# Performance work log

Hardware: AMD Instinct MI355X
Metric: run time of the kernel (lower is better)

Reference implementation:

```python
import jax, jax.numpy as jnp
import numpy as np

EMBED = 256
HEADS = 8
LEVELS = 4
POINTS = 4
HEAD_DIM = EMBED // HEADS
SHAPES = [(100, 100), (50, 50), (25, 25), (13, 13)]  # (H, W) per level
NUM_KEYS = sum(h * w for h, w in SHAPES)  # 13294
LEVEL_STARTS = np.cumsum([0] + [h * w for h, w in SHAPES])[:-1]
B, Q = 8, 900


def _offset_bias():
    # Faithful reproduction of the torch _reset_parameters sampling_offsets bias.
    th = np.arange(HEADS, dtype=np.float32) * (2.0 * np.pi / HEADS)
    g = np.stack([np.cos(th), np.sin(th)], -1)
    g = g / np.abs(g).max(-1, keepdims=True)
    g = np.tile(g[:, None, None, :], (1, LEVELS, POINTS, 1))
    g = g * np.arange(1, POINTS + 1, dtype=np.float32)[None, None, :, None]
    return jnp.asarray(g.reshape(-1), dtype=jnp.float32)


def setup_inputs() -> dict:
    key = jax.random.key(0)
    ks = jax.random.split(key, 12)
    s = 1.0 / np.sqrt(EMBED)
    return {
        "query": jax.random.normal(ks[0], (B, Q, EMBED), jnp.float32),
        "reference_points": jax.random.uniform(ks[1], (B, Q, LEVELS, 2), jnp.float32),
        "value": jax.random.normal(ks[2], (B, NUM_KEYS, EMBED), jnp.float32),
        "spatial_shapes": jnp.asarray(np.array(SHAPES, dtype=np.int32)),
        "level_start_index": jnp.asarray(LEVEL_STARTS.astype(np.int32)),
        "W_off": jax.random.normal(ks[3], (EMBED, HEADS * LEVELS * POINTS * 2), jnp.float32) * 0.01,
        "b_off": _offset_bias(),
        "W_attn": jax.random.normal(ks[4], (EMBED, HEADS * LEVELS * POINTS), jnp.float32) * 0.01,
        "b_attn": jnp.zeros((HEADS * LEVELS * POINTS,), jnp.float32),
        "W_val": jax.random.normal(ks[5], (EMBED, EMBED), jnp.float32) * s,
        "b_val": jnp.zeros((EMBED,), jnp.float32),
        "W_out": jax.random.normal(ks[6], (EMBED, EMBED), jnp.float32) * s,
        "b_out": jnp.zeros((EMBED,), jnp.float32),
    }


def _bilinear(vflat, x, y, H, W):
    # vflat: [BH, H*W, D]; x, y: [BH, Q, P] in unnormalized pixel coords.
    # grid_sample(mode='bilinear', padding_mode='zeros', align_corners=False)
    BH, Qn, Pn = x.shape
    D = vflat.shape[-1]
    x0f = jnp.floor(x); y0f = jnp.floor(y)
    wx = x - x0f; wy = y - y0f
    x0 = x0f.astype(jnp.int32); y0 = y0f.astype(jnp.int32)

    def gather(xi, yi):
        inb = (xi >= 0) & (xi < W) & (yi >= 0) & (yi < H)
        idx = jnp.clip(yi, 0, H - 1) * W + jnp.clip(xi, 0, W - 1)
        g = jnp.take_along_axis(vflat, idx.reshape(BH, Qn * Pn, 1), axis=1)
        return g.reshape(BH, Qn, Pn, D) * inb[..., None].astype(vflat.dtype)

    v00 = gather(x0, y0)
    v01 = gather(x0 + 1, y0)
    v10 = gather(x0, y0 + 1)
    v11 = gather(x0 + 1, y0 + 1)
    return (v00 * ((1 - wx) * (1 - wy))[..., None]
            + v01 * (wx * (1 - wy))[..., None]
            + v10 * ((1 - wx) * wy)[..., None]
            + v11 * (wx * wy)[..., None])


def _msda(value_hd, shapes_np, starts_np, loc, attw):
    # value_hd: [B, K, H, D]; loc: [B, Q, H, L, P, 2]; attw: [B, Q, H, L, P]
    Bn, K, Hn, D = value_hd.shape
    Qn, Pn = loc.shape[1], loc.shape[4]
    out = jnp.zeros((Bn * Hn, Qn, D), value_hd.dtype)
    for l, (Hl, Wl) in enumerate(shapes_np):
        s = int(starts_np[l])
        v = value_hd[:, s:s + Hl * Wl]                      # [B, Hl*Wl, H, D]
        v = v.reshape(Bn, Hl * Wl, Hn, D).transpose(0, 2, 1, 3)
        vflat = v.reshape(Bn * Hn, Hl * Wl, D)
        # sampling_grid = 2*loc - 1; grid_sample align_corners=False -> x = loc*W - 0.5
        lx = loc[:, :, :, l, :, 0].transpose(0, 2, 1, 3).reshape(Bn * Hn, Qn, Pn)
        ly = loc[:, :, :, l, :, 1].transpose(0, 2, 1, 3).reshape(Bn * Hn, Qn, Pn)
        samp = _bilinear(vflat, lx * Wl - 0.5, ly * Hl - 0.5, Hl, Wl)  # [BH,Q,P,D]
        w = attw[:, :, :, l, :].transpose(0, 2, 1, 3).reshape(Bn * Hn, Qn, Pn)
        out = out + jnp.einsum('bqpd,bqp->bqd', samp, w)
    return out.reshape(Bn, Hn, Qn, D).transpose(0, 2, 1, 3).reshape(Bn, Qn, Hn * D)


def reference(query, reference_points, value, spatial_shapes, level_start_index,
              W_off, b_off, W_attn, b_attn, W_val, b_val, W_out, b_out):
    shapes_np = np.asarray(spatial_shapes)
    starts_np = np.asarray(level_start_index)
    Bn, Qn, _ = query.shape
    K = value.shape[1]

    v = value @ W_val + b_val                              # [B, K, E]
    v = v.reshape(Bn, K, HEADS, HEAD_DIM)

    off = (query @ W_off + b_off).reshape(Bn, Qn, HEADS, LEVELS, POINTS, 2)
    aw = (query @ W_attn + b_attn).reshape(Bn, Qn, HEADS, LEVELS * POINTS)
    aw = jax.nn.softmax(aw, axis=-1).reshape(Bn, Qn, HEADS, LEVELS, POINTS)

    # offset_normalizer = (W, H) per level
    norm = jnp.asarray(shapes_np[:, ::-1].astype(np.float32)).reshape(1, 1, 1, LEVELS, 1, 2)
    loc = reference_points[:, :, None, :, None, :] + off / norm  # [B,Q,H,L,P,2]

    out = _msda(v, shapes_np, starts_np, loc, aw)          # [B, Q, E]
    return out @ W_out + b_out
```

## Files before the change

kernel.cpp:

```cpp
#include <hip/hip_runtime.h>
#include <hip/hip_bf16.h>
#include <math.h>
#include <type_traits>

#define BATCH 8
#define QLEN 900
#define HEADS 8
#define LEVELS 4
#define POINTS 4
#define NUM_KEYS 13294
#define BQ (BATCH * QLEN)
#define MROWS_V (BATCH * NUM_KEYS)
#define VTILES (MROWS_V / 16)
#define VBLOCKS 512
#define TPB 13

__constant__ const int c_LH[4] = {100, 50, 25, 13};
__constant__ const int c_LW[4] = {100, 50, 25, 13};
__constant__ const int c_LS[4] = {0, 10000, 12500, 13125};

typedef __attribute__((ext_vector_type(8))) short bfrag;
typedef __attribute__((ext_vector_type(4))) float ffrag;

static __device__ __forceinline__ unsigned short f2bf(float f) {
    __hip_bfloat16 h = __float2bfloat16(f);
    return *(unsigned short*)&h;
}
static __device__ __forceinline__ float bf2f(unsigned int u16) {
    unsigned int v = u16 << 16;
    float f;
    __builtin_memcpy(&f, &v, 4);
    return f;
}
static __device__ __forceinline__ unsigned long long pack4bf(float4 v) {
    return (unsigned long long)f2bf(v.x)
         | ((unsigned long long)f2bf(v.y) << 16)
         | ((unsigned long long)f2bf(v.z) << 32)
         | ((unsigned long long)f2bf(v.w) << 48);
}

__global__ __launch_bounds__(256)
void prep_kernel(const float* __restrict__ W_val, const float* __restrict__ W_off,
                 const float* __restrict__ W_attn, const float* __restrict__ W_out,
                 const float* __restrict__ b_off, const float* __restrict__ b_attn,
                 unsigned short* __restrict__ Wv, unsigned short* __restrict__ Woa,
                 unsigned short* __restrict__ Wo, float* __restrict__ boa) {
    const int id = blockIdx.x * 256 + threadIdx.x;
    if (id < 65536) {
        const int n = id >> 8, k = id & 255;
        Wv[id] = f2bf(W_val[k * 256 + n]);
    } else if (id < 131072) {
        const int t = id - 65536;
        const int n = t >> 8, k = t & 255;
        Woa[t] = f2bf(W_off[k * 256 + n]);
    } else if (id < 163840) {
        const int t = id - 131072;
        const int n = t >> 8, k = t & 255;
        Woa[65536 + t] = f2bf(W_attn[k * 128 + n]);
    } else if (id < 229376) {
        const int t = id - 163840;
        const int n = t >> 8, k = t & 255;
        Wo[t] = f2bf(W_out[k * 256 + n]);
    } else if (id < 229760) {
        const int t = id - 229376;
        boa[t] = (t < 256) ? b_off[t] : b_attn[t - 256];
    }
}

#define VSTEP(T, LREG)                                                        \
  do {                                                                        \
    const char* abuf = (const char*)&Abuf[0][0] + rb * 8192;                  \
    ffrag acc[2];                                                             \
    _Pragma("unroll")                                                         \
    for (int j_ = 0; j_ < 2; ++j_) acc[j_] = (ffrag){0.f, 0.f, 0.f, 0.f};     \
    _Pragma("unroll")                                                         \
    for (int ks_ = 0; ks_ < 8; ++ks_) {                                       \
      const int ub_ = (ks_ * 64 + quad * 16) ^ ((ln & 7) << 4);               \
      const bfrag af_ = *(const bfrag*)(abuf + ln * 512 + ub_);               \
      _Pragma("unroll")                                                       \
      for (int j_ = 0; j_ < 2; ++j_)                                          \
        acc[j_] = __builtin_amdgcn_mfma_f32_16x16x32_bf16(af_, b[j_][ks_],    \
                                                          acc[j_], 0, 0, 0); \
    }                                                                         \
    if ((T) + 1 < t1) {                                                       \
      const int wb_ = (rb + 1 == 3) ? 0 : rb + 1;                             \
      char* dbuf_ = (char*)&Abuf[0][0] + wb_ * 8192;                          \
      _Pragma("unroll")                                                       \
      for (int i_ = 0; i_ < 2; ++i_)                                          \
        *(unsigned long long*)(dbuf_ + dsoff[i_]) = pack4bf(LREG[i_]);        \
      if ((T) + 3 < t1) {                                                     \
        const float4* ap_ = Af4 + (size_t)((T) + 3) * 1024 + tid;             \
        _Pragma("unroll")                                                     \
        for (int i_ = 0; i_ < 2; ++i_) LREG[i_] = ap_[i_ * 512];              \
      }                                                                       \
    }                                                                         \
    const int rowb_ = (T) * 16 + quad * 4;                                    \
    _Pragma("unroll")                                                         \
    for (int r_ = 0; r_ < 4; ++r_) {                                          \
      const unsigned row_ = rowb_ + r_;                                       \
      const unsigned bb_ = row_ / NUM_KEYS;                                   \
      const unsigned key_ = row_ - bb_ * NUM_KEYS;                            \
      _Pragma("unroll")                                                       \
      for (int j_ = 0; j_ < 2; ++j_) {                                        \
        const int col_ = n0 + j_ * 16 + ln;                                   \
        const int h_ = col_ >> 5, d_ = col_ & 31;                             \
        C[((size_t)(bb_ * 8 + h_) * NUM_KEYS + key_) * 32 + d_] =             \
            f2bf(acc[j_][r_] + bj[j_]);                                       \
      }                                                                       \
    }                                                                         \
    asm volatile("s_waitcnt lgkmcnt(0)" ::: "memory");                        \
    __builtin_amdgcn_s_barrier();                                             \
    rb = (rb + 1 == 3) ? 0 : rb + 1;                                          \
  } while (0)

__global__ __launch_bounds__(512, 4)
void gemm_val_stream(const float* __restrict__ A, const unsigned short* __restrict__ WT,
                     const float* __restrict__ bias, unsigned short* __restrict__ C) {
    __shared__ __align__(16) unsigned short Abuf[3][16 * 256];
    const int tid = threadIdx.x;
    const int wave = tid >> 6;
    const int lane = tid & 63;
    const int ln = lane & 15;
    const int quad = lane >> 4;
    const int n0 = wave * 32;

    bfrag b[2][8];
#pragma unroll
    for (int j = 0; j < 2; ++j) {
        const unsigned short* bp = WT + (size_t)(n0 + j * 16 + ln) * 256 + quad * 8;
#pragma unroll
        for (int ks = 0; ks < 8; ++ks) b[j][ks] = *(const bfrag*)(bp + ks * 32);
    }
    float bj[2];
#pragma unroll
    for (int j = 0; j < 2; ++j) bj[j] = bias[n0 + j * 16 + ln];

    const int t0 = blockIdx.x * TPB;
    const int t1 = min(t0 + TPB, VTILES);
    if (t0 >= t1) return;

    int dsoff[2];
#pragma unroll
    for (int i = 0; i < 2; ++i) {
        const int f = i * 512 + tid;
        const int r = f >> 6;
        const int cb = (f & 63) * 8;
        dsoff[i] = r * 512 + (cb ^ ((r & 7) << 4));
    }

    const float4* Af4 = (const float4*)A;

    float4 L0[2], L1[2];
    {
        const float4* ap = Af4 + (size_t)t0 * 1024 + tid;
        float4 P[2];
#pragma unroll
        for (int i = 0; i < 2; ++i) P[i] = ap[i * 512];
#pragma unroll
        for (int i = 0; i < 2; ++i)
            *(unsigned long long*)((char*)&Abuf[0][0] + dsoff[i]) = pack4bf(P[i]);
    }
    if (t0 + 1 < t1) {
        const float4* ap = Af4 + (size_t)(t0 + 1) * 1024 + tid;
#pragma unroll
        for (int i = 0; i < 2; ++i) L0[i] = ap[i * 512];
    }
    if (t0 + 2 < t1) {
        const float4* ap = Af4 + (size_t)(t0 + 2) * 1024 + tid;
#pragma unroll
        for (int i = 0; i < 2; ++i) L1[i] = ap[i * 512];
    }
    asm volatile("s_waitcnt lgkmcnt(0)" ::: "memory");
    __builtin_amdgcn_s_barrier();

    int rb = 0;
    int t = t0;
    while (t + 1 < t1) {
        VSTEP(t, L0);
        VSTEP(t + 1, L1);
        t += 2;
    }
    if (t < t1) VSTEP(t, L0);
}

#define GST 72

template <typename AT, typename CT>
__global__ __launch_bounds__(256)
void gemm_mfma(const AT* __restrict__ A, const unsigned short* __restrict__ WT,
               const float* __restrict__ bias, CT* __restrict__ C,
               int M, int ldc) {
    __shared__ unsigned short As[64 * GST];
    __shared__ unsigned short Bs[128 * GST];
    const int tid = threadIdx.x;
    const int wave = tid >> 6;
    const int lane = tid & 63;
    const int ln = lane & 15;
    const int quad = lane >> 4;
    const int m0 = blockIdx.x * 64;
    const int n0 = blockIdx.y * 128;

    ffrag acc[8];
#pragma unroll
    for (int j = 0; j < 8; ++j) acc[j] = (ffrag){0.f, 0.f, 0.f, 0.f};

    const int ar = tid >> 2;
    const int akc = (tid & 3) * 16;
    const int brow = tid >> 1;
    const int bkc = (tid & 1) * 32;
    const bool a_ok = (m0 + ar) < M;
    const AT* a_src = A + (size_t)(m0 + ar) * 256 + akc;
    const unsigned short* b_src = WT + (size_t)(n0 + brow) * 256 + bkc;

    for (int k0 = 0; k0 < 256; k0 += 64) {
        unsigned short* adst = &As[ar * GST + akc];
        if constexpr (std::is_same<AT, float>::value) {
            float4 f0, f1, f2, f3;
            if (a_ok) {
                const float4* p = (const float4*)(a_src + k0);
                f0 = p[0]; f1 = p[1]; f2 = p[2]; f3 = p[3];
            } else {
                f0 = make_float4(0.f, 0.f, 0.f, 0.f);
                f1 = f0; f2 = f0; f3 = f0;
            }
            float v[16] = {f0.x, f0.y, f0.z, f0.w, f1.x, f1.y, f1.z, f1.w,
                           f2.x, f2.y, f2.z, f2.w, f3.x, f3.y, f3.z, f3.w};
            unsigned short u[16];
#pragma unroll
            for (int i = 0; i < 16; ++i) u[i] = f2bf(v[i]);
            ((uint4*)adst)[0] = ((uint4*)u)[0];
            ((uint4*)adst)[1] = ((uint4*)u)[1];
        } else {
            uint4 u0, u1;
            if (a_ok) {
                const uint4* p = (const uint4*)(a_src + k0);
                u0 = p[0]; u1 = p[1];
            } else {
                u0 = make_uint4(0, 0, 0, 0);
                u1 = u0;
            }
            ((uint4*)adst)[0] = u0;
            ((uint4*)adst)[1] = u1;
        }
        {
            const uint4* src = (const uint4*)(b_src + k0);
            uint4* dst = (uint4*)&Bs[brow * GST + bkc];
#pragma unroll
            for (int i = 0; i < 4; ++i) dst[i] = src[i];
        }
        __syncthreads();

#pragma unroll
        for (int ks = 0; ks < 2; ++ks) {
            const int koff = ks * 32 + quad * 8;
            bfrag af = *(const bfrag*)&As[(wave * 16 + ln) * GST + koff];
#pragma unroll
            for (int j = 0; j < 8; ++j) {
                bfrag bf = *(const bfrag*)&Bs[(j * 16 + ln) * GST + koff];
                acc[j] = __builtin_amdgcn_mfma_f32_16x16x32_bf16(af, bf, acc[j], 0, 0, 0);
            }
        }
        __syncthreads();
    }

#pragma unroll
    for (int j = 0; j < 8; ++j) {
        const int col = n0 + j * 16 + ln;
        const float bb = bias[col];
#pragma unroll
        for (int r = 0; r < 4; ++r) {
            const int row = m0 + wave * 16 + quad * 4 + r;
            if (row < M) {
                const float v = acc[j][r] + bb;
                if constexpr (std::is_same<CT, unsigned short>::value) {
                    C[(size_t)row * ldc + col] = f2bf(v);
                } else {
                    C[(size_t)row * ldc + col] = v;
                }
            }
        }
    }
}

__global__ __launch_bounds__(256, 4)
void msda_sample_kernel(const float* __restrict__ offattn,
                        const float* __restrict__ rp,
                        const unsigned short* __restrict__ vb,
                        unsigned short* __restrict__ outb) {
    const int orig = blockIdx.x;
    const int xcd = orig & 7;
    const int idx = orig >> 3;
    const int wgid = (xcd < 4) ? (xcd * 113 + idx) : (452 + (xcd - 4) * 112 + idx);
    const int hh = wgid / 450;
    const int pos = wgid - hh * 450;
    const int bq0 = pos * 16;
    const int hb = hh * 4;
    const int tid = threadIdx.x;

    __shared__ float s_w[16][64];
    __shared__ float s_x[16][64];
    __shared__ float s_y[16][64];

#pragma unroll
    for (int i = 0; i < 4; ++i) {
        const int e = i * 256 + tid;
        const int q = e >> 6, t = e & 63;
        const int h = hb + (t >> 4), lp = t & 15;
        s_w[q][t] = offattn[(size_t)(bq0 + q) * 384 + 256 + h * 16 + lp];
    }
    __syncthreads();

    if (tid < 64) {
        const int q = tid >> 2, h4 = tid & 3;
        float m = -1e30f;
#pragma unroll
        for (int i = 0; i < 16; ++i) m = fmaxf(m, s_w[q][h4 * 16 + i]);
        float e[16];
        float ssum = 0.f;
#pragma unroll
        for (int i = 0; i < 16; ++i) {
            e[i] = expf(s_w[q][h4 * 16 + i] - m);
            ssum += e[i];
        }
        const float inv = 1.f / ssum;
#pragma unroll
        for (int i = 0; i < 16; ++i) s_w[q][h4 * 16 + i] = e[i] * inv;
    }

#pragma unroll
    for (int i = 0; i < 4; ++i) {
        const int e = i * 256 + tid;
        const int q = e >> 6, t = e & 63;
        const int h = hb + (t >> 4), l = (t >> 2) & 3, p = t & 3;
        const int bq = bq0 + q;
        const float2 off = *(const float2*)(offattn + (size_t)bq * 384 + h * 32 + l * 8 + p * 2);
        const float Wl = (float)c_LW[l];
        const float Hl = (float)c_LH[l];
        const float rx = rp[((size_t)bq * 4 + l) * 2 + 0];
        const float ry = rp[((size_t)bq * 4 + l) * 2 + 1];
        s_x[q][t] = (rx + off.x / Wl) * Wl - 0.5f;
        s_y[q][t] = (ry + off.y / Hl) * Hl - 0.5f;
    }
    __syncthreads();

    const int q = tid >> 4;
    const int s = tid & 15;
    const int h4 = s >> 2;
    const int dp = s & 3;
    const int bq = bq0 + q;
    const int b = bq / QLEN;
    const int h = hb + h4;
    const unsigned short* vbase = vb + (size_t)(b * 8 + h) * NUM_KEYS * 32 + dp * 8;

    float acc[8];
#pragma unroll
    for (int d = 0; d < 8; ++d) acc[d] = 0.f;

#pragma unroll
    for (int l = 0; l < LEVELS; ++l) {
        const int Hl = c_LH[l];
        const int Wl = c_LW[l];
        const int s0 = c_LS[l];
#pragma unroll 2
        for (int p = 0; p < POINTS; ++p) {
            const int t2 = h4 * 16 + l * 4 + p;
            const float x = s_x[q][t2];
            const float y = s_y[q][t2];
            const float w = s_w[q][t2];
            const float x0f = floorf(x);
            const float y0f = floorf(y);
            const float wx = x - x0f;
            const float wy = y - y0f;
            const int x0 = (int)x0f;
            const int y0 = (int)y0f;
            const float mx0 = ((unsigned)x0 < (unsigned)Wl) ? 1.f : 0.f;
            const float mx1 = ((unsigned)(x0 + 1) < (unsigned)Wl) ? 1.f : 0.f;
            const float my0 = ((unsigned)y0 < (unsigned)Hl) ? 1.f : 0.f;
            const float my1 = ((unsigned)(y0 + 1) < (unsigned)Hl) ? 1.f : 0.f;
            const int xc0 = min(max(x0, 0), Wl - 1);
            const int xc1 = min(max(x0 + 1, 0), Wl - 1);
            const int yc0 = min(max(y0, 0), Hl - 1);
            const int yc1 = min(max(y0 + 1, 0), Hl - 1);
            const float a00 = w * (1.f - wx) * (1.f - wy) * mx0 * my0;
            const float a01 = w * wx * (1.f - wy) * mx1 * my0;
            const float a10 = w * (1.f - wx) * wy * mx0 * my1;
            const float a11 = w * wx * wy * mx1 * my1;
            const size_t k00 = (size_t)(s0 + yc0 * Wl + xc0) * 32;
            const size_t k01 = (size_t)(s0 + yc0 * Wl + xc1) * 32;
            const size_t k10 = (size_t)(s0 + yc1 * Wl + xc0) * 32;
            const size_t k11 = (size_t)(s0 + yc1 * Wl + xc1) * 32;
            const uint4 r00 = *(const uint4*)(vbase + k00);
            const uint4 r01 = *(const uint4*)(vbase + k01);
            const uint4 r10 = *(const uint4*)(vbase + k10);
            const uint4 r11 = *(const uint4*)(vbase + k11);
            const unsigned int w00[4] = {r00.x, r00.y, r00.z, r00.w};
            const unsigned int w01[4] = {r01.x, r01.y, r01.z, r01.w};
            const unsigned int w10[4] = {r10.x, r10.y, r10.z, r10.w};
            const unsigned int w11[4] = {r11.x, r11.y, r11.z, r11.w};
#pragma unroll
            for (int i = 0; i < 4; ++i) {
                const float v00l = bf2f(w00[i] & 0xffffu), v00h = bf2f(w00[i] >> 16);
                const float v01l = bf2f(w01[i] & 0xffffu), v01h = bf2f(w01[i] >> 16);
                const float v10l = bf2f(w10[i] & 0xffffu), v10h = bf2f(w10[i] >> 16);
                const float v11l = bf2f(w11[i] & 0xffffu), v11h = bf2f(w11[i] >> 16);
                acc[i * 2 + 0] = fmaf(a00, v00l, fmaf(a01, v01l, fmaf(a10, v10l, fmaf(a11, v11l, acc[i * 2 + 0]))));
                acc[i * 2 + 1] = fmaf(a00, v00h, fmaf(a01, v01h, fmaf(a10, v10h, fmaf(a11, v11h, acc[i * 2 + 1]))));
            }
        }
    }

    unsigned short o[8];
#pragma unroll
    for (int d = 0; d < 8; ++d) o[d] = f2bf(acc[d]);
    *(uint4*)(outb + (size_t)bq * 256 + h * 32 + dp * 8) = *(uint4*)o;
}

extern "C" void kernel_launch(void* const* d_in, const int* in_sizes, int n_in,
                              void* d_out, int out_size, void* d_ws, size_t ws_size,
                              hipStream_t stream) {
    const float* query  = (const float*)d_in[0];
    const float* rp     = (const float*)d_in[1];
    const float* value  = (const float*)d_in[2];
    const float* W_off  = (const float*)d_in[5];
    const float* b_off  = (const float*)d_in[6];
    const float* W_attn = (const float*)d_in[7];
    const float* b_attn = (const float*)d_in[8];
    const float* W_val  = (const float*)d_in[9];
    const float* b_val  = (const float*)d_in[10];
    const float* W_out  = (const float*)d_in[11];
    const float* b_out  = (const float*)d_in[12];
    float* out = (float*)d_out;

    char* w = (char*)d_ws;
    unsigned short* ws_vb = (unsigned short*)w;
    w += (size_t)MROWS_V * 256 * 2;
    float* ws_offattn = (float*)w;
    w += (size_t)BQ * 384 * 4;
    unsigned short* ws_msda = (unsigned short*)w;
    w += (size_t)BQ * 256 * 2;
    unsigned short* ws_Wv = (unsigned short*)w;  w += 256 * 256 * 2;
    unsigned short* ws_Woa = (unsigned short*)w; w += 384 * 256 * 2;
    unsigned short* ws_Wo = (unsigned short*)w;  w += 256 * 256 * 2;
    float* ws_boa = (float*)w;

    prep_kernel<<<898, 256, 0, stream>>>(W_val, W_off, W_attn, W_out,
                                         b_off, b_attn, ws_Wv, ws_Woa, ws_Wo, ws_boa);

    gemm_val_stream<<<VBLOCKS, 512, 0, stream>>>(value, ws_Wv, b_val, ws_vb);

    {
        dim3 grid((BQ + 63) / 64, 3);
        gemm_mfma<float, float><<<grid, 256, 0, stream>>>(
            query, ws_Woa, ws_boa, ws_offattn, BQ, 384);
    }
    msda_sample_kernel<<<900, 256, 0, stream>>>(ws_offattn, rp, ws_vb, ws_msda);

    {
        dim3 grid((BQ + 63) / 64, 2);
        gemm_mfma<unsigned short, float><<<grid, 256, 0, stream>>>(
            ws_msda, ws_Wo, b_out, out, BQ, 256);
    }
}
```

Measured before the change: 244.7 us.

## Stream value-projection A tiles straight to LDS with global_load_lds

The streaming value-projection GEMM used to load fp32 A tiles into registers, pack them to bf16 and write them to LDS. It now uses async global_load_lds to copy the fp32 rows straight into a swizzled triple-buffered LDS ring and converts to bf16 when building the MFMA fragments. This is meant to remove the register staging and the extra VGPR pressure, and to let the loads overlap compute through vmcnt-based waits. In exchange LDS use per block doubles, which may cut blocks per CU, LDS read traffic doubles, and the conversion work moves into the inner loop.

```diff
diff --git a/kernel.cpp b/kernel.cpp
--- a/kernel.cpp
+++ b/kernel.cpp
@@ -32,11 +32,11 @@
     __builtin_memcpy(&f, &v, 4);
     return f;
 }
-static __device__ __forceinline__ unsigned long long pack4bf(float4 v) {
-    return (unsigned long long)f2bf(v.x)
-         | ((unsigned long long)f2bf(v.y) << 16)
-         | ((unsigned long long)f2bf(v.z) << 32)
-         | ((unsigned long long)f2bf(v.w) << 48);
+
+typedef __attribute__((address_space(1))) void* as1_vp;
+typedef __attribute__((address_space(3))) void* as3_vp;
+static __device__ __forceinline__ void gload16(const void* g, void* l) {
+    __builtin_amdgcn_global_load_lds((as1_vp)(void*)g, (as3_vp)l, 16, 0, 0);
 }
 
 __global__ __launch_bounds__(256)
@@ -67,56 +67,10 @@
     }
 }
 
-#define VSTEP(T, LREG)                                                        \
-  do {                                                                        \
-    const char* abuf = (const char*)&Abuf[0][0] + rb * 8192;                  \
-    ffrag acc[2];                                                             \
-    _Pragma("unroll")                                                         \
-    for (int j_ = 0; j_ < 2; ++j_) acc[j_] = (ffrag){0.f, 0.f, 0.f, 0.f};     \
-    _Pragma("unroll")                                                         \
-    for (int ks_ = 0; ks_ < 8; ++ks_) {                                       \
-      const int ub_ = (ks_ * 64 + quad * 16) ^ ((ln & 7) << 4);               \
-      const bfrag af_ = *(const bfrag*)(abuf + ln * 512 + ub_);               \
-      _Pragma("unroll")                                                       \
-      for (int j_ = 0; j_ < 2; ++j_)                                          \
-        acc[j_] = __builtin_amdgcn_mfma_f32_16x16x32_bf16(af_, b[j_][ks_],    \
-                                                          acc[j_], 0, 0, 0); \
-    }                                                                         \
-    if ((T) + 1 < t1) {                                                       \
-      const int wb_ = (rb + 1 == 3) ? 0 : rb + 1;                             \
-      char* dbuf_ = (char*)&Abuf[0][0] + wb_ * 8192;                          \
-      _Pragma("unroll")                                                       \
-      for (int i_ = 0; i_ < 2; ++i_)                                          \
-        *(unsigned long long*)(dbuf_ + dsoff[i_]) = pack4bf(LREG[i_]);        \
-      if ((T) + 3 < t1) {                                                     \
-        const float4* ap_ = Af4 + (size_t)((T) + 3) * 1024 + tid;             \
-        _Pragma("unroll")                                                     \
-        for (int i_ = 0; i_ < 2; ++i_) LREG[i_] = ap_[i_ * 512];              \
-      }                                                                       \
-    }                                                                         \
-    const int rowb_ = (T) * 16 + quad * 4;                                    \
-    _Pragma("unroll")                                                         \
-    for (int r_ = 0; r_ < 4; ++r_) {                                          \
-      const unsigned row_ = rowb_ + r_;                                       \
-      const unsigned bb_ = row_ / NUM_KEYS;                                   \
-      const unsigned key_ = row_ - bb_ * NUM_KEYS;                            \
-      _Pragma("unroll")                                                       \
-      for (int j_ = 0; j_ < 2; ++j_) {                                        \
-        const int col_ = n0 + j_ * 16 + ln;                                   \
-        const int h_ = col_ >> 5, d_ = col_ & 31;                             \
-        C[((size_t)(bb_ * 8 + h_) * NUM_KEYS + key_) * 32 + d_] =             \
-            f2bf(acc[j_][r_] + bj[j_]);                                       \
-      }                                                                       \
-    }                                                                         \
-    asm volatile("s_waitcnt lgkmcnt(0)" ::: "memory");                        \
-    __builtin_amdgcn_s_barrier();                                             \
-    rb = (rb + 1 == 3) ? 0 : rb + 1;                                          \
-  } while (0)
-
 __global__ __launch_bounds__(512, 4)
 void gemm_val_stream(const float* __restrict__ A, const unsigned short* __restrict__ WT,
                      const float* __restrict__ bias, unsigned short* __restrict__ C) {
-    __shared__ __align__(16) unsigned short Abuf[3][16 * 256];
+    __shared__ __align__(16) float Abuf[3][16 * 256];
     const int tid = threadIdx.x;
     const int wave = tid >> 6;
     const int lane = tid & 63;
@@ -139,48 +93,72 @@
     const int t1 = min(t0 + TPB, VTILES);
     if (t0 >= t1) return;
 
-    int dsoff[2];
+    int goff[2], loff[2];
 #pragma unroll
     for (int i = 0; i < 2; ++i) {
-        const int f = i * 512 + tid;
-        const int r = f >> 6;
-        const int cb = (f & 63) * 8;
-        dsoff[i] = r * 512 + (cb ^ ((r & 7) << 4));
-    }
-
-    const float4* Af4 = (const float4*)A;
-
-    float4 L0[2], L1[2];
-    {
-        const float4* ap = Af4 + (size_t)t0 * 1024 + tid;
-        float4 P[2];
-#pragma unroll
-        for (int i = 0; i < 2; ++i) P[i] = ap[i * 512];
+        const int j = wave * 2 + i;
+        goff[i] = j * 1024 + ((lane ^ (j & 7)) << 4);
+        loff[i] = j * 1024;
+    }
+
+    const char* Ab = (const char*)A;
+    char* lds0 = (char*)&Abuf[0][0];
+
+#pragma unroll
+    for (int i = 0; i < 2; ++i)
+        gload16(Ab + (size_t)t0 * 16384 + goff[i], lds0 + loff[i]);
+    if (t0 + 1 < t1) {
 #pragma unroll
         for (int i = 0; i < 2; ++i)
-            *(unsigned long long*)((char*)&Abuf[0][0] + dsoff[i]) = pack4bf(P[i]);
-    }
-    if (t0 + 1 < t1) {
-        const float4* ap = Af4 + (size_t)(t0 + 1) * 1024 + tid;
-#pragma unroll
-        for (int i = 0; i < 2; ++i) L0[i] = ap[i * 512];
-    }
-    if (t0 + 2 < t1) {
-        const float4* ap = Af4 + (size_t)(t0 + 2) * 1024 + tid;
-#pragma unroll
-        for (int i = 0; i < 2; ++i) L1[i] = ap[i * 512];
-    }
-    asm volatile("s_waitcnt lgkmcnt(0)" ::: "memory");
+            gload16(Ab + (size_t)(t0 + 1) * 16384 + goff[i], lds0 + 16384 + loff[i]);
+    }
+    asm volatile("s_waitcnt vmcnt(2)" ::: "memory");
     __builtin_amdgcn_s_barrier();
 
     int rb = 0;
-    int t = t0;
-    while (t + 1 < t1) {
-        VSTEP(t, L0);
-        VSTEP(t + 1, L1);
-        t += 2;
-    }
-    if (t < t1) VSTEP(t, L0);
+    for (int t = t0; t < t1; ++t) {
+        const char* abuf = lds0 + rb * 16384;
+        ffrag acc[2];
+#pragma unroll
+        for (int j = 0; j < 2; ++j) acc[j] = (ffrag){0.f, 0.f, 0.f, 0.f};
+#pragma unroll
+        for (int ks = 0; ks < 8; ++ks) {
+            const int c0 = ks * 8 + quad * 2;
+            const float4 f0 = *(const float4*)(abuf + ln * 1024 + ((c0 ^ (ln & 7)) << 4));
+            const float4 f1 = *(const float4*)(abuf + ln * 1024 + (((c0 + 1) ^ (ln & 7)) << 4));
+            unsigned short u[8] = {f2bf(f0.x), f2bf(f0.y), f2bf(f0.z), f2bf(f0.w),
+                                   f2bf(f1.x), f2bf(f1.y), f2bf(f1.z), f2bf(f1.w)};
+            const bfrag af = *(const bfrag*)u;
+            acc[0] = __builtin_amdgcn_mfma_f32_16x16x32_bf16(af, b[0][ks], acc[0], 0, 0, 0);
+            acc[1] = __builtin_amdgcn_mfma_f32_16x16x32_bf16(af, b[1][ks], acc[1], 0, 0, 0);
+        }
+
+        if (t + 2 < t1) {
+            char* dbuf = lds0 + ((rb + 2 >= 3) ? rb - 1 : rb + 2) * 16384;
+#pragma unroll
+            for (int i = 0; i < 2; ++i)
+                gload16(Ab + (size_t)(t + 2) * 16384 + goff[i], dbuf + loff[i]);
+        }
+
+        const int rowb = t * 16 + quad * 4;
+#pragma unroll
+        for (int r = 0; r < 4; ++r) {
+            const unsigned row = rowb + r;
+            const unsigned bb = row / NUM_KEYS;
+            const unsigned key = row - bb * NUM_KEYS;
+#pragma unroll
+            for (int j = 0; j < 2; ++j) {
+                const int col = n0 + j * 16 + ln;
+                const int h = col >> 5, d = col & 31;
+                C[((size_t)(bb * 8 + h) * NUM_KEYS + key) * 32 + d] =
+                    f2bf(acc[j][r] + bj[j]);
+            }
+        }
+
+        asm volatile("s_waitcnt vmcnt(10)" ::: "memory");
+        __builtin_amdgcn_s_barrier();
+        rb = (rb + 1 == 3) ? 0 : rb + 1;
+    }
 }
 
 #define GST 72
```

Result: no change. 247.6 us (+1.2%).
